# Optimization experiments

Hardware: AMD Instinct MI355X
Metric: run time of the kernel (lower is better)

Reference implementation:

```python
import jax, jax.numpy as jnp
import numpy as np

IN_DIM = 3
OUT_DIM = 3
HIDDEN = [40, 40, 40, 40, 40, 40]
N_POINTS = 2_097_152


def _glorot(key, fan_in, fan_out):
    std = jnp.sqrt(2.0 / (fan_in + fan_out)).astype(jnp.float32)
    return jax.random.normal(key, (fan_in, fan_out), dtype=jnp.float32) * std


def setup_inputs() -> dict:
    key = jax.random.key(0)
    keys = jax.random.split(key, 8)
    coords = jax.random.uniform(keys[0], (N_POINTS, IN_DIM), dtype=jnp.float32)
    dims = [IN_DIM] + HIDDEN + [OUT_DIM]  # [3,40,40,40,40,40,40,3]
    inp = {"coords": coords}
    for i in range(7):
        inp[f"W{i}"] = _glorot(keys[i + 1], dims[i], dims[i + 1])
        inp[f"b{i}"] = jnp.zeros((dims[i + 1],), dtype=jnp.float32)
    return inp


def reference(coords, W0, b0, W1, b1, W2, b2, W3, b3, W4, b4, W5, b5, W6, b6):
    # 7-layer coordinate MLP: Linear+Tanh x6, final Linear. coords: [N,3] -> [N,3]
    Ws = [W0, W1, W2, W3, W4, W5, W6]
    bs = [b0, b1, b2, b3, b4, b5, b6]
    x = coords
    for i in range(6):
        x = jnp.tanh(x @ Ws[i] + bs[i])
    return x @ Ws[6] + bs[6]
```

## Files before the change

kernel.cpp:

```cpp
#include <hip/hip_runtime.h>


typedef _Float16 f16x8 __attribute__((ext_vector_type(8)));
typedef float    f32x16 __attribute__((ext_vector_type(16)));
typedef unsigned int u32x4 __attribute__((ext_vector_type(4)));

#define NFRAG  35
#define TABN   225
#define TABREP 32
#define SEXP   2
#define INVH   32.0f
#define UOFF   112.0f
#define UMAX   223.999f
#define TABR   3.5f
#define EXPSC  2.8853900817779268f

__constant__ int INV[48] = {
     0,  1,  2,  3,   8,  9, 10, 11,   4,  5,  6,  7,  12, 13, 14, 15,
    16, 17, 18, 19,  24, 25, 26, 27,  20, 21, 22, 23,  28, 29, 30, 31,
    32, 33, 34, 35,  -1, -1, -1, -1,  36, 37, 38, 39,  -2, -3, -1, -1 };

__constant__ int KAP[40] = {
     0,  1,  2,  3,   8,  9, 10, 11,   4,  5,  6,  7,  12, 13, 14, 15,
    16, 17, 18, 19,  24, 25, 26, 27,  20, 21, 22, 23,  28, 29, 30, 31,
    32, 33, 34, 35,  40, 41, 42, 43 };

__global__ void prep_frags(const float* __restrict__ W0, const float* __restrict__ b0,
                           const float* __restrict__ W1, const float* __restrict__ b1,
                           const float* __restrict__ W2, const float* __restrict__ b2,
                           const float* __restrict__ W3, const float* __restrict__ b3,
                           const float* __restrict__ W4, const float* __restrict__ b4,
                           const float* __restrict__ W5, const float* __restrict__ b5,
                           const float* __restrict__ W6, const float* __restrict__ b6,
                           unsigned short* __restrict__ frags,
                           unsigned* __restrict__ table)
{
    int tid = blockIdx.x * 256 + threadIdx.x;

    if (tid < NFRAG * 64) {
        int frag = tid >> 6, lane = tid & 63;

        int layer, mt, ch;
        if (frag < 2)       { layer = 0; mt = frag; ch = 0; }
        else if (frag < 32) { int t = frag - 2; layer = 1 + t / 6; int r = t % 6; mt = r / 3; ch = r % 3; }
        else                { layer = 6; mt = 0; ch = frag - 32; }

        const float* Ws[7] = { W0, W1, W2, W3, W4, W5, W6 };
        const float* bs[7] = { b0, b1, b2, b3, b4, b5, b6 };
        const float* W = Ws[layer];
        const float* b = bs[layer];
        const int fout = (layer == 6) ? 3 : 40;

        int jout  = mt * 32 + (lane & 31);
        int kbase = ch * 16 + (lane >> 5) * 8;

        unsigned short h[8];
        for (int i = 0; i < 8; ++i) {
            int k = kbase + i;
            float v = 0.0f;
            if (jout < fout) {
                int jin;
                if (layer == 0) jin = (k < 3) ? k : ((k == 3) ? -2 : ((k == 4) ? -3 : -1));
                else            jin = INV[k];
                bool ex = false;
                if (layer < 6) {
                    int kp = KAP[jout];
                    int P = 4 * (kp >> 4) + ((kp & 7) >> 1);
                    ex = (P < SEXP);
                }
                float scale = (layer == 6) ? 1.0f : (ex ? EXPSC : INVH);
                if (jin >= 0)       v = W[jin * fout + jout] * scale;
                else if (jin == -2) v = b[jout] * scale;
                else if (jin == -3) v = (layer == 6 || ex) ? 0.0f : UOFF;
            }
            _Float16 hv = (_Float16)v;
            h[i] = __builtin_bit_cast(unsigned short, hv);
        }
        unsigned short* dst = frags + frag * 512 + lane * 8;
        for (int i = 0; i < 8; ++i) dst[i] = h[i];
    }
    else if (tid < NFRAG * 64 + TABN) {
        int i = tid - NFRAG * 64;
        const float H = 1.0f / 32.0f;
        float x  = -TABR + (float)i * H;
        float t0 = tanhf(x);
        float t1 = tanhf(x + H);
        float MID = 0.5f * (1.0f + tanhf(TABR));
        float base = t0, delta = t1 - t0;
        if (i == 0)        { base = -MID; delta = t1 - base; }
        if (i == TABN - 2) { delta = MID - t0; }
        unsigned short bb = __builtin_bit_cast(unsigned short, (_Float16)base);
        unsigned short dd = __builtin_bit_cast(unsigned short, (_Float16)delta);
        table[i] = (unsigned)bb | ((unsigned)dd << 16);
    }
}

__device__ __forceinline__ unsigned int pkf16(float a, float b) {
    return __builtin_bit_cast(unsigned int, __builtin_amdgcn_cvt_pkrtz(a, b));
}
__device__ __forceinline__ f32x16 zf() {
    f32x16 v;
    #pragma unroll
    for (int i = 0; i < 16; ++i) v[i] = 0.0f;
    return v;
}
__device__ __forceinline__ float exp2_fast(float y) {
#if __has_builtin(__builtin_amdgcn_exp2f)
    return __builtin_amdgcn_exp2f(y);
#else
    float e;
    asm("v_exp_f32 %0, %1" : "=v"(e) : "v"(y));
    return e;
#endif
}
__device__ __forceinline__ f16x8 mkf(unsigned a, unsigned b, unsigned c, unsigned d) {
    u32x4 t = { a, b, c, d };
    return __builtin_bit_cast(f16x8, t);
}

#define MFMA __builtin_amdgcn_mfma_f32_32x32x16_f16

struct BfT { unsigned w0, w1, w2, w3, w4, w5, w6, w7, w8, w9, w10, w11; };

#define BFC0(B) mkf((B).w0, (B).w1, (B).w2,  (B).w3)
#define BFC1(B) mkf((B).w4, (B).w5, (B).w6,  (B).w7)
#define BFC2(B) mkf((B).w8, (B).w9, (B).w10, (B).w11)

#define ACT_D1(Db, B) do {                            \
    (B).w8  = tl2(Db[0],  Db[1]);                     \
    (B).w9  = tl2(Db[2],  Db[3]);                     \
    (B).w10 = PK11;                                   \
    (B).w11 = 0u;                                     \
} while (0)

#define ACT_D0(Da, B) do {                            \
    (B).w0  = pkf16(te(Da[0]),  te(Da[1]));           \
    (B).w1  = pkf16(te(Da[2]),  te(Da[3]));           \
    (B).w2  = tl2(Da[4],  Da[5]);                     \
    (B).w3  = tl2(Da[6],  Da[7]);                     \
    (B).w4  = tl2(Da[8],  Da[9]);                     \
    (B).w5  = tl2(Da[10], Da[11]);                    \
    (B).w6  = tl2(Da[12], Da[13]);                    \
    (B).w7  = tl2(Da[14], Da[15]);                    \
} while (0)

#define L0_TILE(B) do {                               \
    f16x8 bb = BFC0(B);                               \
    {                                                 \
        f32x16 D1 = MFMA(F1, bb, CZ, 0, 0, 0);        \
        ACT_D1(D1, B);                                \
    }                                                 \
    {                                                 \
        f32x16 D0 = MFMA(F0, bb, CZ, 0, 0, 0);        \
        ACT_D0(D0, B);                                \
    }                                                 \
} while (0)

#define HID_TILE(B) do {                              \
    f16x8 B0 = BFC0(B), B1 = BFC1(B), B2 = BFC2(B);   \
    {                                                 \
        f32x16 D1 = MFMA(F3, B0, CZ, 0, 0, 0);        \
        D1 = MFMA(F4, B1, D1, 0, 0, 0);               \
        D1 = MFMA(F5, B2, D1, 0, 0, 0);               \
        ACT_D1(D1, B);                                \
    }                                                 \
    {                                                 \
        f32x16 D0 = MFMA(F0, B0, CZ, 0, 0, 0);        \
        D0 = MFMA(F1, B1, D0, 0, 0, 0);               \
        D0 = MFMA(F2, B2, D0, 0, 0, 0);               \
        ACT_D0(D0, B);                                \
    }                                                 \
} while (0)

#define FIN_TILE(B, pX, vX) do {                      \
    f32x16 D0 = MFMA(F0, BFC0(B), CZ, 0, 0, 0);       \
    D0 = MFMA(F1, BFC1(B), D0, 0, 0, 0);              \
    D0 = MFMA(F2, BFC2(B), D0, 0, 0, 0);              \
    if (lane < 32 && vX) {                            \
        out[(pX) * 3 + 0] = D0[0];                    \
        out[(pX) * 3 + 1] = D0[1];                    \
        out[(pX) * 3 + 2] = D0[2];                    \
    }                                                 \
} while (0)

__global__ __launch_bounds__(512) void mlp_mfma(const float* __restrict__ coords,
                                                const unsigned short* __restrict__ frags,
                                                const unsigned* __restrict__ gtab,
                                                float* __restrict__ out, int npts)
{
    __shared__ __align__(16) unsigned stab[TABN * TABREP];
    {
        for (int i = threadIdx.x; i < TABN * TABREP; i += 512) stab[i] = gtab[i >> 5];
    }
    __syncthreads();

    const int lane = threadIdx.x & 63;
    const int wid  = threadIdx.x >> 6;
    const int pA   = (blockIdx.x * 8 + wid) * 64 + (lane & 31);
    const int pB   = pA + 32;
    const bool vA = (pA < npts), vB = (pB < npts);

    const unsigned int PK11 = pkf16(1.0f, 1.0f);
    const unsigned* __restrict__ tb = stab + (lane & 31);
    const f32x16 CZ = zf();

    auto tl2 = [&](float ua, float ub) -> unsigned {
        ua = __builtin_amdgcn_fmed3f(ua, 0.0f, UMAX);
        ub = __builtin_amdgcn_fmed3f(ub, 0.0f, UMAX);
        float fa = __builtin_amdgcn_fractf(ua);
        float fb = __builtin_amdgcn_fractf(ub);
        unsigned ea = tb[(unsigned)ua * TABREP];
        unsigned eb = tb[(unsigned)ub * TABREP];
        unsigned r;
        asm("v_fma_mixlo_f16 %0, %1, %2, %2 op_sel:[0,1,0] op_sel_hi:[0,1,1]"
            : "=v"(r) : "v"(fa), "v"(ea));
        asm("v_fma_mixhi_f16 %0, %1, %2, %2 op_sel:[0,1,0] op_sel_hi:[0,1,1]"
            : "+v"(r) : "v"(fb), "v"(eb));
        return r;
    };
    auto te = [&](float y) -> float {
        float e = exp2_fast(y);
        float r = __builtin_amdgcn_rcpf(e + 1.0f);
        return __builtin_fmaf(-2.0f, r, 1.0f);
    };

    BfT A, B;
    {
        float a0 = 0.f, a1 = 0.f, a2 = 0.f, b0 = 0.f, b1 = 0.f, b2 = 0.f;
        if (vA) { a0 = coords[pA * 3]; a1 = coords[pA * 3 + 1]; a2 = coords[pA * 3 + 2]; }
        if (vB) { b0 = coords[pB * 3]; b1 = coords[pB * 3 + 1]; b2 = coords[pB * 3 + 2]; }
        A.w0 = pkf16(a0, a1); A.w1 = pkf16(a2, 1.0f);
        B.w0 = pkf16(b0, b1); B.w1 = pkf16(b2, 1.0f);
        A.w2 = B.w2 = pkf16(1.0f, 0.0f);
        A.w3 = B.w3 = 0u;
    }

    auto AF = [&](int f) -> f16x8 {
        return ((const f16x8*)frags)[f * 64 + lane];
    };

    f16x8 F0, F1, F2, F3, F4, F5;

    F0 = AF(0); F1 = AF(1);
    L0_TILE(A); L0_TILE(B);

    #pragma unroll
    for (int l = 1; l <= 5; ++l) {
        const int fb = 2 + (l - 1) * 6;
        F0 = AF(fb + 0); F1 = AF(fb + 1); F2 = AF(fb + 2);
        F3 = AF(fb + 3); F4 = AF(fb + 4); F5 = AF(fb + 5);
        HID_TILE(A); HID_TILE(B);
    }

    F0 = AF(32); F1 = AF(33); F2 = AF(34);
    FIN_TILE(A, pA, vA);
    FIN_TILE(B, pB, vB);
}

extern "C" void kernel_launch(void* const* d_in, const int* in_sizes, int n_in,
                              void* d_out, int out_size, void* d_ws, size_t ws_size,
                              hipStream_t stream)
{
    const float* coords = (const float*)d_in[0];
    const float* W0 = (const float*)d_in[1];  const float* b0 = (const float*)d_in[2];
    const float* W1 = (const float*)d_in[3];  const float* b1 = (const float*)d_in[4];
    const float* W2 = (const float*)d_in[5];  const float* b2 = (const float*)d_in[6];
    const float* W3 = (const float*)d_in[7];  const float* b3 = (const float*)d_in[8];
    const float* W4 = (const float*)d_in[9];  const float* b4 = (const float*)d_in[10];
    const float* W5 = (const float*)d_in[11]; const float* b5 = (const float*)d_in[12];
    const float* W6 = (const float*)d_in[13]; const float* b6 = (const float*)d_in[14];
    float* out = (float*)d_out;

    unsigned short* frags = (unsigned short*)d_ws;
    unsigned* table = (unsigned*)((char*)d_ws + NFRAG * 1024);

    const int npts = in_sizes[0] / 3;

    const int prep_threads = NFRAG * 64 + TABN;
    prep_frags<<<(prep_threads + 255) / 256, 256, 0, stream>>>(
        W0, b0, W1, b1, W2, b2, W3, b3, W4, b4, W5, b5, W6, b6, frags, table);

    const int blocks = (npts + 511) / 512;
    mlp_mfma<<<blocks, 512, 0, stream>>>(coords, frags, table, out, npts);
}
```

Baseline: 116.0 us.

## Replace LDS tanh lookup table with exp2/rcp tanh for all neurons

Removes the hybrid activation scheme in which most hidden neurons used a shared-memory piecewise-linear tanh table and only a few used exp2+rcp. Every neuron now uses the transcendental formula, with all weights pre-scaled by 2/ln2. This drops the LDS table, its fill loop and the block barrier. Blocks shrink from 512 to 256 threads. The trade is more work on the transcendental unit (exp and rcp per element) in place of LDS gathers and FMA-mix interpolation, which was probably there to balance load across the two units.

```diff
diff --git a/kernel.cpp b/kernel.cpp
--- a/kernel.cpp
+++ b/kernel.cpp
@@ -6,24 +6,12 @@
 typedef unsigned int u32x4 __attribute__((ext_vector_type(4)));
 
 #define NFRAG  35
-#define TABN   225
-#define TABREP 32
-#define SEXP   2
-#define INVH   32.0f
-#define UOFF   112.0f
-#define UMAX   223.999f
-#define TABR   3.5f
 #define EXPSC  2.8853900817779268f
 
 __constant__ int INV[48] = {
      0,  1,  2,  3,   8,  9, 10, 11,   4,  5,  6,  7,  12, 13, 14, 15,
     16, 17, 18, 19,  24, 25, 26, 27,  20, 21, 22, 23,  28, 29, 30, 31,
-    32, 33, 34, 35,  -1, -1, -1, -1,  36, 37, 38, 39,  -2, -3, -1, -1 };
-
-__constant__ int KAP[40] = {
-     0,  1,  2,  3,   8,  9, 10, 11,   4,  5,  6,  7,  12, 13, 14, 15,
-    16, 17, 18, 19,  24, 25, 26, 27,  20, 21, 22, 23,  28, 29, 30, 31,
-    32, 33, 34, 35,  40, 41, 42, 43 };
+    32, 33, 34, 35,  -1, -1, -1, -1,  36, 37, 38, 39,  -2, -1, -1, -1 };
 
 __global__ void prep_frags(const float* __restrict__ W0, const float* __restrict__ b0,
                            const float* __restrict__ W1, const float* __restrict__ b1,
@@ -32,67 +20,44 @@
                            const float* __restrict__ W4, const float* __restrict__ b4,
                            const float* __restrict__ W5, const float* __restrict__ b5,
                            const float* __restrict__ W6, const float* __restrict__ b6,
-                           unsigned short* __restrict__ frags,
-                           unsigned* __restrict__ table)
+                           unsigned short* __restrict__ frags)
 {
     int tid = blockIdx.x * 256 + threadIdx.x;
-
-    if (tid < NFRAG * 64) {
-        int frag = tid >> 6, lane = tid & 63;
-
-        int layer, mt, ch;
-        if (frag < 2)       { layer = 0; mt = frag; ch = 0; }
-        else if (frag < 32) { int t = frag - 2; layer = 1 + t / 6; int r = t % 6; mt = r / 3; ch = r % 3; }
-        else                { layer = 6; mt = 0; ch = frag - 32; }
-
-        const float* Ws[7] = { W0, W1, W2, W3, W4, W5, W6 };
-        const float* bs[7] = { b0, b1, b2, b3, b4, b5, b6 };
-        const float* W = Ws[layer];
-        const float* b = bs[layer];
-        const int fout = (layer == 6) ? 3 : 40;
-
-        int jout  = mt * 32 + (lane & 31);
-        int kbase = ch * 16 + (lane >> 5) * 8;
-
-        unsigned short h[8];
-        for (int i = 0; i < 8; ++i) {
-            int k = kbase + i;
-            float v = 0.0f;
-            if (jout < fout) {
-                int jin;
-                if (layer == 0) jin = (k < 3) ? k : ((k == 3) ? -2 : ((k == 4) ? -3 : -1));
-                else            jin = INV[k];
-                bool ex = false;
-                if (layer < 6) {
-                    int kp = KAP[jout];
-                    int P = 4 * (kp >> 4) + ((kp & 7) >> 1);
-                    ex = (P < SEXP);
-                }
-                float scale = (layer == 6) ? 1.0f : (ex ? EXPSC : INVH);
-                if (jin >= 0)       v = W[jin * fout + jout] * scale;
-                else if (jin == -2) v = b[jout] * scale;
-                else if (jin == -3) v = (layer == 6 || ex) ? 0.0f : UOFF;
-            }
-            _Float16 hv = (_Float16)v;
-            h[i] = __builtin_bit_cast(unsigned short, hv);
+    if (tid >= NFRAG * 64) return;
+
+    int frag = tid >> 6, lane = tid & 63;
+
+    int layer, mt, ch;
+    if (frag < 2)       { layer = 0; mt = frag; ch = 0; }
+    else if (frag < 32) { int t = frag - 2; layer = 1 + t / 6; int r = t % 6; mt = r / 3; ch = r % 3; }
+    else                { layer = 6; mt = 0; ch = frag - 32; }
+
+    const float* Ws[7] = { W0, W1, W2, W3, W4, W5, W6 };
+    const float* bs[7] = { b0, b1, b2, b3, b4, b5, b6 };
+    const float* W = Ws[layer];
+    const float* b = bs[layer];
+    const int fout = (layer == 6) ? 3 : 40;
+    const float scale = (layer == 6) ? 1.0f : EXPSC;
+
+    int jout  = mt * 32 + (lane & 31);
+    int kbase = ch * 16 + (lane >> 5) * 8;
+
+    unsigned short h[8];
+    for (int i = 0; i < 8; ++i) {
+        int k = kbase + i;
+        float v = 0.0f;
+        if (jout < fout) {
+            int jin;
+            if (layer == 0) jin = (k < 3) ? k : ((k == 3) ? -2 : -1);
+            else            jin = INV[k];
+            if (jin >= 0)       v = W[jin * fout + jout] * scale;
+            else if (jin == -2) v = b[jout] * scale;
         }
-        unsigned short* dst = frags + frag * 512 + lane * 8;
-        for (int i = 0; i < 8; ++i) dst[i] = h[i];
+        _Float16 hv = (_Float16)v;
+        h[i] = __builtin_bit_cast(unsigned short, hv);
     }
-    else if (tid < NFRAG * 64 + TABN) {
-        int i = tid - NFRAG * 64;
-        const float H = 1.0f / 32.0f;
-        float x  = -TABR + (float)i * H;
-        float t0 = tanhf(x);
-        float t1 = tanhf(x + H);
-        float MID = 0.5f * (1.0f + tanhf(TABR));
-        float base = t0, delta = t1 - t0;
-        if (i == 0)        { base = -MID; delta = t1 - base; }
-        if (i == TABN - 2) { delta = MID - t0; }
-        unsigned short bb = __builtin_bit_cast(unsigned short, (_Float16)base);
-        unsigned short dd = __builtin_bit_cast(unsigned short, (_Float16)delta);
-        table[i] = (unsigned)bb | ((unsigned)dd << 16);
-    }
+    unsigned short* dst = frags + frag * 512 + lane * 8;
+    for (int i = 0; i < 8; ++i) dst[i] = h[i];
 }
 
 __device__ __forceinline__ unsigned int pkf16(float a, float b) {
@@ -127,21 +92,21 @@
 #define BFC2(B) mkf((B).w8, (B).w9, (B).w10, (B).w11)
 
 #define ACT_D1(Db, B) do {                            \
-    (B).w8  = tl2(Db[0],  Db[1]);                     \
-    (B).w9  = tl2(Db[2],  Db[3]);                     \
+    (B).w8  = pkf16(te(Db[0]), te(Db[1]));            \
+    (B).w9  = pkf16(te(Db[2]), te(Db[3]));            \
     (B).w10 = PK11;                                   \
     (B).w11 = 0u;                                     \
 } while (0)
 
 #define ACT_D0(Da, B) do {                            \
-    (B).w0  = pkf16(te(Da[0]),  te(Da[1]));           \
-    (B).w1  = pkf16(te(Da[2]),  te(Da[3]));           \
-    (B).w2  = tl2(Da[4],  Da[5]);                     \
-    (B).w3  = tl2(Da[6],  Da[7]);                     \
-    (B).w4  = tl2(Da[8],  Da[9]);                     \
-    (B).w5  = tl2(Da[10], Da[11]);                    \
-    (B).w6  = tl2(Da[12], Da[13]);                    \
-    (B).w7  = tl2(Da[14], Da[15]);                    \
+    (B).w0 = pkf16(te(Da[0]),  te(Da[1]));            \
+    (B).w1 = pkf16(te(Da[2]),  te(Da[3]));            \
+    (B).w2 = pkf16(te(Da[4]),  te(Da[5]));            \
+    (B).w3 = pkf16(te(Da[6]),  te(Da[7]));            \
+    (B).w4 = pkf16(te(Da[8]),  te(Da[9]));            \
+    (B).w5 = pkf16(te(Da[10]), te(Da[11]));           \
+    (B).w6 = pkf16(te(Da[12]), te(Da[13]));           \
+    (B).w7 = pkf16(te(Da[14]), te(Da[15]));           \
 } while (0)
 
 #define L0_TILE(B) do {                               \
@@ -183,41 +148,19 @@
     }                                                 \
 } while (0)
 
-__global__ __launch_bounds__(512) void mlp_mfma(const float* __restrict__ coords,
+__global__ __launch_bounds__(256) void mlp_mfma(const float* __restrict__ coords,
                                                 const unsigned short* __restrict__ frags,
-                                                const unsigned* __restrict__ gtab,
                                                 float* __restrict__ out, int npts)
 {
-    __shared__ __align__(16) unsigned stab[TABN * TABREP];
-    {
-        for (int i = threadIdx.x; i < TABN * TABREP; i += 512) stab[i] = gtab[i >> 5];
-    }
-    __syncthreads();
-
     const int lane = threadIdx.x & 63;
     const int wid  = threadIdx.x >> 6;
-    const int pA   = (blockIdx.x * 8 + wid) * 64 + (lane & 31);
+    const int pA   = (blockIdx.x * 4 + wid) * 64 + (lane & 31);
     const int pB   = pA + 32;
     const bool vA = (pA < npts), vB = (pB < npts);
 
     const unsigned int PK11 = pkf16(1.0f, 1.0f);
-    const unsigned* __restrict__ tb = stab + (lane & 31);
     const f32x16 CZ = zf();
 
-    auto tl2 = [&](float ua, float ub) -> unsigned {
-        ua = __builtin_amdgcn_fmed3f(ua, 0.0f, UMAX);
-        ub = __builtin_amdgcn_fmed3f(ub, 0.0f, UMAX);
-        float fa = __builtin_amdgcn_fractf(ua);
-        float fb = __builtin_amdgcn_fractf(ub);
-        unsigned ea = tb[(unsigned)ua * TABREP];
-        unsigned eb = tb[(unsigned)ub * TABREP];
-        unsigned r;
-        asm("v_fma_mixlo_f16 %0, %1, %2, %2 op_sel:[0,1,0] op_sel_hi:[0,1,1]"
-            : "=v"(r) : "v"(fa), "v"(ea));
-        asm("v_fma_mixhi_f16 %0, %1, %2, %2 op_sel:[0,1,0] op_sel_hi:[0,1,1]"
-            : "+v"(r) : "v"(fb), "v"(eb));
-        return r;
-    };
     auto te = [&](float y) -> float {
         float e = exp2_fast(y);
         float r = __builtin_amdgcn_rcpf(e + 1.0f);
@@ -231,7 +174,7 @@
         if (vB) { b0 = coords[pB * 3]; b1 = coords[pB * 3 + 1]; b2 = coords[pB * 3 + 2]; }
         A.w0 = pkf16(a0, a1); A.w1 = pkf16(a2, 1.0f);
         B.w0 = pkf16(b0, b1); B.w1 = pkf16(b2, 1.0f);
-        A.w2 = B.w2 = pkf16(1.0f, 0.0f);
+        A.w2 = B.w2 = 0u;
         A.w3 = B.w3 = 0u;
     }
 
@@ -272,14 +215,12 @@
     float* out = (float*)d_out;
 
     unsigned short* frags = (unsigned short*)d_ws;
-    unsigned* table = (unsigned*)((char*)d_ws + NFRAG * 1024);
 
     const int npts = in_sizes[0] / 3;
 
-    const int prep_threads = NFRAG * 64 + TABN;
-    prep_frags<<<(prep_threads + 255) / 256, 256, 0, stream>>>(
-        W0, b0, W1, b1, W2, b2, W3, b3, W4, b4, W5, b5, W6, b6, frags, table);
-
-    const int blocks = (npts + 511) / 512;
-    mlp_mfma<<<blocks, 512, 0, stream>>>(coords, frags, table, out, npts);
-}
+    prep_frags<<<(NFRAG * 64 + 255) / 256, 256, 0, stream>>>(
+        W0, b0, W1, b1, W2, b2, W3, b3, W4, b4, W5, b5, W6, b6, frags);
+
+    const int blocks = (npts + 255) / 256;
+    mlp_mfma<<<blocks, 256, 0, stream>>>(coords, frags, out, npts);
+}
```

Result: slower. 121.0 us (+4.3%).
